# Optimization experiments

Measured on AMD Instinct MI355X. Metric: run time of the kernel, lower is better.

## Reference

```python
import jax, jax.numpy as jnp
import numpy as np

EMB, DK, DV = 768, 256, 256
B, N = 8, 2048


def setup_inputs() -> dict:
    key = jax.random.key(0)
    ks = jax.random.split(key, 9)
    s = 1.0 / np.sqrt(EMB)
    # Stack the 3 per-head Linear layers into [3, EMB, D] weights (same math).
    Wq = jax.random.uniform(ks[0], (3, EMB, DK), jnp.float32, -s, s)
    bq = jax.random.uniform(ks[1], (3, DK), jnp.float32, -s, s)
    Wk = jax.random.uniform(ks[2], (3, EMB, DK), jnp.float32, -s, s)
    bk = jax.random.uniform(ks[3], (3, DK), jnp.float32, -s, s)
    Wv = jax.random.uniform(ks[4], (3, EMB, DV), jnp.float32, -s, s)
    bv = jax.random.uniform(ks[5], (3, DV), jnp.float32, -s, s)
    s0 = 1.0 / np.sqrt(3 * DV)
    W0 = jax.random.uniform(ks[6], (3 * DV, EMB), jnp.float32, -s0, s0)
    b0 = jax.random.uniform(ks[7], (EMB,), jnp.float32, -s0, s0)
    x = jax.random.normal(ks[8], (B, N, EMB), jnp.float32)
    return {"x": x, "Wq": Wq, "bq": bq, "Wk": Wk, "bk": bk,
            "Wv": Wv, "bv": bv, "W0": W0, "b0": b0}


def reference(x, Wq, bq, Wk, bk, Wv, bv, W0, b0):
    # QKV for all 3 heads in one batched GEMM each: [B,3,N,D]
    Q = jnp.einsum('bne,hed->bhnd', x, Wq) + bq[None, :, None, :]
    K = jnp.einsum('bne,hed->bhnd', x, Wk) + bk[None, :, None, :]
    V = jnp.einsum('bne,hed->bhnd', x, Wv) + bv[None, :, None, :]
    scores = jnp.einsum('bhnd,bhmd->bhnm', Q, K) / jnp.sqrt(jnp.float32(DK))
    attn = jax.nn.softmax(scores, axis=-1)
    res = jnp.einsum('bhnm,bhmd->bhnd', attn, V)  # [B,3,N,DV]
    # concat heads along feature dim (head order matches torch concat order)
    res = jnp.transpose(res, (0, 2, 1, 3)).reshape(B, N, 3 * DV)
    return res @ W0 + b0
```

## Files before the change

### kernel.cpp

```cpp
#include <hip/hip_runtime.h>
#include <stdint.h>

typedef __attribute__((ext_vector_type(8))) short short8;
typedef __attribute__((ext_vector_type(4))) float floatx4;

#define EMB 768
#define DKV 256
#define NB  8
#define NS  2048

__device__ __forceinline__ float b2f(unsigned short u) {
  union { unsigned int i; float f; } v; v.i = ((unsigned int)u) << 16; return v.f;
}
__device__ __forceinline__ unsigned short f2b(float f) {
  union { float f; unsigned int i; } v; v.f = f;
  return (unsigned short)((v.i + 0x7FFFu + ((v.i >> 16) & 1u)) >> 16);
}

__device__ __forceinline__ short8 load8x(const void* p, size_t e, int f32) {
  short8 r;
  if (f32) {
    const float* f = (const float*)p + e;
    float4 a = *(const float4*)f;
    float4 b = *(const float4*)(f + 4);
    r[0] = (short)f2b(a.x); r[1] = (short)f2b(a.y);
    r[2] = (short)f2b(a.z); r[3] = (short)f2b(a.w);
    r[4] = (short)f2b(b.x); r[5] = (short)f2b(b.y);
    r[6] = (short)f2b(b.z); r[7] = (short)f2b(b.w);
  } else {
    r = *(const short8*)((const unsigned short*)p + e);
  }
  return r;
}
__device__ __forceinline__ float loadf(const void* p, size_t e, int f32) {
  return f32 ? ((const float*)p)[e] : b2f(((const unsigned short*)p)[e]);
}

__global__ __launch_bounds__(256) void detect_kernel(
    const unsigned short* __restrict__ x, int* __restrict__ flag) {
  __shared__ int cnt;
  if (threadIdx.x == 0) cnt = 0;
  __syncthreads();
  int bad = 0;
  for (int i = threadIdx.x; i < 1024; i += 256) {
    float v = b2f(x[i]);
    if (!(fabsf(v) <= 1e4f)) bad++;
  }
  atomicAdd(&cnt, bad);
  __syncthreads();
  if (threadIdx.x == 0) flag[0] = (cnt > 16) ? 1 : 0;
}

__global__ __launch_bounds__(256) void repack_wt(
    const void* __restrict__ Wq, const void* __restrict__ Wk,
    const void* __restrict__ Wv, unsigned short* __restrict__ WT,
    const int* __restrict__ flag) {
  __shared__ unsigned short tile[32][33];
  const int f32 = *flag;
  const int tid = threadIdx.x;
  const int slab = blockIdx.z;
  const int t = slab / 3, h = slab - t * 3;
  const int k0 = blockIdx.x * 32, d0 = blockIdx.y * 32;
  const void* Wsrc = (t == 0) ? Wq : ((t == 1) ? Wk : Wv);
#pragma unroll
  for (int rr = 0; rr < 4; ++rr) {
    int ki = rr * 8 + (tid >> 5), di = tid & 31;
    tile[ki][di] = f2b(loadf(Wsrc, (size_t)(h * EMB + k0 + ki) * DKV + d0 + di, f32));
  }
  __syncthreads();
#pragma unroll
  for (int rr = 0; rr < 4; ++rr) {
    int di = rr * 8 + (tid >> 5), ki = tid & 31;
    WT[(size_t)(slab * 256 + d0 + di) * EMB + k0 + ki] = tile[ki][di];
  }
}

__global__ __launch_bounds__(256) void repack_w0t(
    const void* __restrict__ W0, unsigned short* __restrict__ W0T,
    const int* __restrict__ flag) {
  __shared__ unsigned short tile[32][33];
  const int f32 = *flag;
  const int tid = threadIdx.x;
  const int k0 = blockIdx.x * 32, o0 = blockIdx.y * 32;
#pragma unroll
  for (int rr = 0; rr < 4; ++rr) {
    int ki = rr * 8 + (tid >> 5), oi = tid & 31;
    tile[ki][oi] = f2b(loadf(W0, (size_t)(k0 + ki) * EMB + o0 + oi, f32));
  }
  __syncthreads();
#pragma unroll
  for (int rr = 0; rr < 4; ++rr) {
    int oi = rr * 8 + (tid >> 5), ki = tid & 31;
    W0T[(size_t)(o0 + oi) * EMB + k0 + ki] = tile[ki][oi];
  }
}

__global__ __launch_bounds__(256, 2) void kv_gemm(
    const void* __restrict__ X, const unsigned short* __restrict__ WT,
    const void* __restrict__ bk, const void* __restrict__ bv,
    unsigned short* __restrict__ Kb, unsigned short* __restrict__ Vtb,
    const int* __restrict__ flag) {
  __shared__ __align__(16) unsigned short As[128 * 40];
  __shared__ __align__(16) unsigned short BsK[128 * 40];
  __shared__ __align__(16) unsigned short BsV[128 * 40];
  const int f32 = *flag;
  const int tid = threadIdx.x;
  const int wave = tid >> 6, lane = tid & 63, quad = lane >> 4, l15 = lane & 15;
  const int wm = wave >> 1, wn = wave & 1;
  const int row0 = blockIdx.y * 128;
  const int cb = blockIdx.x * 128;

  floatx4 accK[4][4], accV[4][4];
  for (int m = 0; m < 4; ++m)
    for (int n = 0; n < 4; ++n) { accK[m][n] = (floatx4)0.0f; accV[m][n] = (floatx4)0.0f; }

  const size_t arow0 = (size_t)row0 * EMB;
  const unsigned short* BbK = WT + (size_t)(768 + cb) * EMB;
  const unsigned short* BbV = WT + (size_t)(1536 + cb) * EMB;

  for (int k0 = 0; k0 < EMB; k0 += 32) {
    short8 va[2], vk[2], vv[2];
#pragma unroll
    for (int i = 0; i < 2; ++i) {
      int idx = i * 256 + tid;
      int r = idx >> 2, kp = (idx & 3) << 3;
      va[i] = load8x(X, arow0 + (size_t)r * EMB + k0 + kp, f32);
      vk[i] = *(const short8*)(BbK + (size_t)r * EMB + k0 + kp);
      vv[i] = *(const short8*)(BbV + (size_t)r * EMB + k0 + kp);
    }
    __syncthreads();
#pragma unroll
    for (int i = 0; i < 2; ++i) {
      int idx = i * 256 + tid;
      int off = (idx >> 2) * 40 + (idx & 3) * 8;
      *(short8*)&As[off] = va[i];
      *(short8*)&BsK[off] = vk[i];
      *(short8*)&BsV[off] = vv[i];
    }
    __syncthreads();
    short8 af[4], bk4[4], bv4[4];
#pragma unroll
    for (int m = 0; m < 4; ++m)
      af[m] = *(const short8*)&As[(wm * 64 + m * 16 + l15) * 40 + quad * 8];
#pragma unroll
    for (int n = 0; n < 4; ++n) {
      bk4[n] = *(const short8*)&BsK[(wn * 64 + n * 16 + l15) * 40 + quad * 8];
      bv4[n] = *(const short8*)&BsV[(wn * 64 + n * 16 + l15) * 40 + quad * 8];
    }
#pragma unroll
    for (int n = 0; n < 4; ++n)
#pragma unroll
      for (int m = 0; m < 4; ++m) {
        accK[m][n] = __builtin_amdgcn_mfma_f32_16x16x32_bf16(af[m], bk4[n], accK[m][n], 0, 0, 0);
        accV[m][n] = __builtin_amdgcn_mfma_f32_16x16x32_bf16(af[m], bv4[n], accV[m][n], 0, 0, 0);
      }
  }

  const int h = cb >> 8;
  const int dbase = cb & 255;

#pragma unroll
  for (int n = 0; n < 4; ++n) {
    const int cc = wn * 64 + n * 16 + l15;
    const float bvv = loadf(bk, h * 256 + dbase + cc, f32);
    const int d = dbase + cc;
#pragma unroll
    for (int m = 0; m < 4; ++m) {
      const int rbase = row0 + wm * 64 + m * 16 + quad * 4;
#pragma unroll
      for (int r = 0; r < 4; ++r) {
        const int row = rbase + r;
        const int bb = row >> 11, nn = row & 2047;
        Kb[((size_t)(bb * 3 + h) * 2048 + nn) * 256 + d] = f2b(accK[m][n][r] + bvv);
      }
    }
  }
#pragma unroll
  for (int n = 0; n < 4; ++n) {
    const int cc = wn * 64 + n * 16 + l15;
    const float bvv = loadf(bv, h * 256 + dbase + cc, f32);
    const int d = dbase + cc;
#pragma unroll
    for (int m = 0; m < 4; ++m) {
      const int rbase = row0 + wm * 64 + m * 16 + quad * 4;
      const int bb = rbase >> 11, nn = rbase & 2047;
      const size_t base = ((size_t)(bb * 3 + h) * 256 + d) * 2048 + nn;
      uint2 val;
      val.x = (uint32_t)f2b(accV[m][n][0] + bvv) | ((uint32_t)f2b(accV[m][n][1] + bvv) << 16);
      val.y = (uint32_t)f2b(accV[m][n][2] + bvv) | ((uint32_t)f2b(accV[m][n][3] + bvv) << 16);
      *(uint2*)(Vtb + base) = val;
    }
  }
}

__global__ __launch_bounds__(256, 3) void flash_fused(
    const void* __restrict__ X, const unsigned short* __restrict__ WT,
    const void* __restrict__ bq,
    const unsigned short* __restrict__ Kb, const unsigned short* __restrict__ Vtb,
    unsigned short* __restrict__ Ob, const int* __restrict__ flag) {
  __shared__ __align__(16) unsigned short smem[21248];
  unsigned short* AsQ = smem;
  unsigned short* BsQ = smem + 2560;
  unsigned short* Qs  = smem;
  unsigned short* Ks  = smem;
  unsigned short* Vts = smem + 8448;
  unsigned short* Ps  = smem + 18688;

  const int f32 = *flag;
  const int tid = threadIdx.x;
  const int wave = tid >> 6, lane = tid & 63, quad = lane >> 4, l15 = lane & 15;
  const int bh = blockIdx.x;
  const int bb = bh / 3, hh = bh - bb * 3;
  const int q0 = blockIdx.y * 64;

  short8 qf[8];

  {
    const size_t xrow0 = (size_t)bb * NS + q0;
    floatx4 qacc[4][4];
    for (int m = 0; m < 4; ++m)
      for (int n = 0; n < 4; ++n) qacc[m][n] = (floatx4)0.0f;

    for (int k0 = 0; k0 < EMB; k0 += 32) {
      short8 va, vb[4];
      {
        int r = tid >> 2, kp = (tid & 3) << 3;
        va = load8x(X, (xrow0 + r) * EMB + k0 + kp, f32);
      }
#pragma unroll
      for (int i = 0; i < 4; ++i) {
        int c = i * 256 + tid;
        int n = c >> 2, kp = (c & 3) << 3;
        vb[i] = *(const short8*)(WT + (size_t)(hh * 256 + n) * EMB + k0 + kp);
      }
      __syncthreads();
      *(short8*)&AsQ[(tid >> 2) * 40 + (tid & 3) * 8] = va;
#pragma unroll
      for (int i = 0; i < 4; ++i) {
        int c = i * 256 + tid;
        *(short8*)&BsQ[(c >> 2) * 40 + (c & 3) * 8] = vb[i];
      }
      __syncthreads();
      short8 af[4], bf[4];
#pragma unroll
      for (int m = 0; m < 4; ++m)
        af[m] = *(const short8*)&AsQ[(m * 16 + l15) * 40 + quad * 8];
#pragma unroll
      for (int n = 0; n < 4; ++n)
        bf[n] = *(const short8*)&BsQ[(wave * 64 + n * 16 + l15) * 40 + quad * 8];
#pragma unroll
      for (int n = 0; n < 4; ++n)
#pragma unroll
        for (int m = 0; m < 4; ++m)
          qacc[m][n] = __builtin_amdgcn_mfma_f32_16x16x32_bf16(af[m], bf[n], qacc[m][n], 0, 0, 0);
    }
    __syncthreads();

#pragma unroll
    for (int n = 0; n < 4; ++n) {
      const int col = wave * 64 + n * 16 + l15;
      const float bqv = loadf(bq, hh * 256 + col, f32);
#pragma unroll
      for (int m = 0; m < 4; ++m)
#pragma unroll
        for (int r = 0; r < 4; ++r)
          Qs[(m * 16 + quad * 4 + r) * 264 + col] = f2b((qacc[m][n][r] + bqv) * 0.0625f);
    }
    __syncthreads();
#pragma unroll
    for (int ks = 0; ks < 8; ++ks)
      qf[ks] = *(const short8*)&Qs[(wave * 16 + l15) * 264 + ks * 32 + quad * 8];
    __syncthreads();
  }

  const unsigned short* Kp = Kb + (size_t)bh * NS * DKV;
  const unsigned short* Vp = Vtb + (size_t)bh * DKV * NS;

  floatx4 oacc[4][4];
  for (int m = 0; m < 4; ++m)
    for (int ct = 0; ct < 4; ++ct) oacc[m][ct] = (floatx4)0.0f;
  float l_part[4] = {0.f, 0.f, 0.f, 0.f};

  for (int j0 = 0; j0 < NS; j0 += 32) {
    short8 kv[4], vv[4];
#pragma unroll
    for (int i = 0; i < 4; ++i) {
      int c = i * 256 + tid;
      kv[i] = *(const short8*)(Kp + (size_t)(j0 + (c >> 5)) * DKV + ((c & 31) << 3));
      vv[i] = *(const short8*)(Vp + (size_t)(c >> 2) * NS + j0 + ((c & 3) << 3));
    }
    __syncthreads();
#pragma unroll
    for (int i = 0; i < 4; ++i) {
      int c = i * 256 + tid;
      *(short8*)&Ks[(c >> 5) * 264 + (c & 31) * 8] = kv[i];
      *(short8*)&Vts[(c >> 2) * 40 + (c & 3) * 8] = vv[i];
    }
    __syncthreads();

    floatx4 sacc[2];
    sacc[0] = (floatx4)0.0f; sacc[1] = (floatx4)0.0f;
    __builtin_amdgcn_s_setprio(1);
#pragma unroll
    for (int ks = 0; ks < 8; ++ks)
#pragma unroll
      for (int ct = 0; ct < 2; ++ct) {
        short8 bfr = *(const short8*)&Ks[(ct * 16 + l15) * 264 + ks * 32 + quad * 8];
        sacc[ct] = __builtin_amdgcn_mfma_f32_16x16x32_bf16(qf[ks], bfr, sacc[ct], 0, 0, 0);
      }
    __builtin_amdgcn_s_setprio(0);

#pragma unroll
    for (int ct = 0; ct < 2; ++ct)
#pragma unroll
      for (int r = 0; r < 4; ++r) {
        float p = __expf(sacc[ct][r]);
        l_part[r] += p;
        Ps[(wave * 16 + quad * 4 + r) * 40 + ct * 16 + l15] = f2b(p);
      }
    __syncthreads();

    short8 pa[4];
#pragma unroll
    for (int m = 0; m < 4; ++m)
      pa[m] = *(const short8*)&Ps[(m * 16 + l15) * 40 + quad * 8];
    __builtin_amdgcn_s_setprio(1);
#pragma unroll
    for (int ct = 0; ct < 4; ++ct) {
      short8 vb = *(const short8*)&Vts[(wave * 64 + ct * 16 + l15) * 40 + quad * 8];
#pragma unroll
      for (int m = 0; m < 4; ++m)
        oacc[m][ct] = __builtin_amdgcn_mfma_f32_16x16x32_bf16(pa[m], vb, oacc[m][ct], 0, 0, 0);
    }
    __builtin_amdgcn_s_setprio(0);
  }

  float l_r[4];
#pragma unroll
  for (int r = 0; r < 4; ++r) l_r[r] = l_part[r];
#pragma unroll
  for (int mask = 1; mask < 16; mask <<= 1)
#pragma unroll
    for (int r = 0; r < 4; ++r) l_r[r] += __shfl_xor(l_r[r], mask);

  __syncthreads();
  float* Lsf = (float*)smem;
  if (l15 == 0) {
#pragma unroll
    for (int r = 0; r < 4; ++r) Lsf[wave * 16 + quad * 4 + r] = l_r[r];
  }
  __syncthreads();

#pragma unroll
  for (int m = 0; m < 4; ++m) {
    float linv[4];
#pragma unroll
    for (int r = 0; r < 4; ++r) linv[r] = 1.0f / Lsf[m * 16 + quad * 4 + r];
#pragma unroll
    for (int ct = 0; ct < 4; ++ct) {
      const int col = hh * DKV + wave * 64 + ct * 16 + l15;
#pragma unroll
      for (int r = 0; r < 4; ++r) {
        const int n = q0 + m * 16 + quad * 4 + r;
        Ob[((size_t)(bb * NS + n)) * EMB + col] = f2b(oacc[m][ct][r] * linv[r]);
      }
    }
  }
}

__global__ __launch_bounds__(256) void out_gemm(
    const unsigned short* __restrict__ A, const unsigned short* __restrict__ W0T,
    const void* __restrict__ b0, void* __restrict__ out,
    const int* __restrict__ flag) {
  __shared__ __align__(16) unsigned short As[128 * 40];
  __shared__ __align__(16) unsigned short Bs[128 * 40];
  const int f32 = *flag;
  const int tid = threadIdx.x;
  const int wave = tid >> 6, lane = tid & 63, quad = lane >> 4, l15 = lane & 15;
  const int wm = wave >> 1, wn = wave & 1;
  const int row0 = blockIdx.y * 128;
  const int c0 = blockIdx.x * 128;

  floatx4 acc[4][4];
  for (int m = 0; m < 4; ++m)
    for (int n = 0; n < 4; ++n) acc[m][n] = (floatx4)0.0f;

  const unsigned short* Ab = A + (size_t)row0 * EMB;
  const unsigned short* Bb = W0T + (size_t)c0 * EMB;

  for (int k0 = 0; k0 < EMB; k0 += 32) {
    short8 va[2], vb[2];
#pragma unroll
    for (int i = 0; i < 2; ++i) {
      int idx = i * 256 + tid;
      int r = idx >> 2, kp = (idx & 3) << 3;
      va[i] = *(const short8*)(Ab + (size_t)r * EMB + k0 + kp);
      vb[i] = *(const short8*)(Bb + (size_t)r * EMB + k0 + kp);
    }
    __syncthreads();
#pragma unroll
    for (int i = 0; i < 2; ++i) {
      int idx = i * 256 + tid;
      *(short8*)&As[(idx >> 2) * 40 + (idx & 3) * 8] = va[i];
      *(short8*)&Bs[(idx >> 2) * 40 + (idx & 3) * 8] = vb[i];
    }
    __syncthreads();
    short8 af[4], bf[4];
#pragma unroll
    for (int m = 0; m < 4; ++m)
      af[m] = *(const short8*)&As[(wm * 64 + m * 16 + l15) * 40 + quad * 8];
#pragma unroll
    for (int n = 0; n < 4; ++n)
      bf[n] = *(const short8*)&Bs[(wn * 64 + n * 16 + l15) * 40 + quad * 8];
#pragma unroll
    for (int n = 0; n < 4; ++n)
#pragma unroll
      for (int m = 0; m < 4; ++m)
        acc[m][n] = __builtin_amdgcn_mfma_f32_16x16x32_bf16(af[m], bf[n], acc[m][n], 0, 0, 0);
  }

#pragma unroll
  for (int n = 0; n < 4; ++n) {
    const int col = c0 + wn * 64 + n * 16 + l15;
    const float bvv = loadf(b0, col, f32);
#pragma unroll
    for (int m = 0; m < 4; ++m) {
      const int rbase = row0 + wm * 64 + m * 16 + quad * 4;
#pragma unroll
      for (int r = 0; r < 4; ++r) {
        const float v = acc[m][n][r] + bvv;
        const size_t idx = (size_t)(rbase + r) * EMB + col;
        if (f32) ((float*)out)[idx] = v;
        else     ((unsigned short*)out)[idx] = f2b(v);
      }
    }
  }
}

extern "C" void kernel_launch(void* const* d_in, const int* in_sizes, int n_in,
                              void* d_out, int out_size, void* d_ws, size_t ws_size,
                              hipStream_t stream) {
  const void* x  = d_in[0];
  const void* Wq = d_in[1];
  const void* bq = d_in[2];
  const void* Wk = d_in[3];
  const void* bk = d_in[4];
  const void* Wv = d_in[5];
  const void* bv = d_in[6];
  const void* W0 = d_in[7];
  const void* b0 = d_in[8];

  unsigned short* ws = (unsigned short*)d_ws;
  const size_t SZ = (size_t)NB * 3 * NS * DKV;
  unsigned short* Kb  = (unsigned short*)d_out;
  unsigned short* Vtb = ws;
  unsigned short* Ob  = ws + SZ;
  unsigned short* WT  = ws + 2 * SZ;
  unsigned short* W0T = WT + (size_t)2304 * EMB;
  int* flag = (int*)(W0T + (size_t)EMB * EMB);

  detect_kernel<<<dim3(1), dim3(256), 0, stream>>>((const unsigned short*)x, flag);
  repack_wt<<<dim3(24, 8, 9), dim3(256), 0, stream>>>(Wq, Wk, Wv, WT, flag);
  repack_w0t<<<dim3(24, 24), dim3(256), 0, stream>>>(W0, W0T, flag);
  kv_gemm<<<dim3(6, 128), dim3(256), 0, stream>>>(x, WT, bk, bv, Kb, Vtb, flag);
  flash_fused<<<dim3(24, 32), dim3(256), 0, stream>>>(x, WT, bq, Kb, Vtb, Ob, flag);
  out_gemm<<<dim3(6, 128), dim3(256), 0, stream>>>(Ob, W0T, b0, d_out, flag);
}
```

Before: 449.1 us.

## Prefetch next K-tile into registers across all GEMM and attention loops

Applies register double-buffering to the KV projection GEMM, the Q projection, the attention K/V streaming loop and the output projection. Each loop now issues global loads for the next tile right after storing the current tile to LDS, so memory latency overlaps with the MFMA work. The attention loop moves its barrier to the end of each iteration so LDS is not overwritten early. It also raises wave priority around MFMA blocks. This costs extra live registers, which may lower occupancy.

```diff
diff --git a/kernel.cpp b/kernel.cpp
--- a/kernel.cpp
+++ b/kernel.cpp
@@ -118,16 +118,17 @@
   const unsigned short* BbK = WT + (size_t)(768 + cb) * EMB;
   const unsigned short* BbV = WT + (size_t)(1536 + cb) * EMB;
 
+  short8 va[2], vk[2], vv[2];
+#pragma unroll
+  for (int i = 0; i < 2; ++i) {
+    int idx = i * 256 + tid;
+    int r = idx >> 2, kp = (idx & 3) << 3;
+    va[i] = load8x(X, arow0 + (size_t)r * EMB + kp, f32);
+    vk[i] = *(const short8*)(BbK + (size_t)r * EMB + kp);
+    vv[i] = *(const short8*)(BbV + (size_t)r * EMB + kp);
+  }
+
   for (int k0 = 0; k0 < EMB; k0 += 32) {
-    short8 va[2], vk[2], vv[2];
-#pragma unroll
-    for (int i = 0; i < 2; ++i) {
-      int idx = i * 256 + tid;
-      int r = idx >> 2, kp = (idx & 3) << 3;
-      va[i] = load8x(X, arow0 + (size_t)r * EMB + k0 + kp, f32);
-      vk[i] = *(const short8*)(BbK + (size_t)r * EMB + k0 + kp);
-      vv[i] = *(const short8*)(BbV + (size_t)r * EMB + k0 + kp);
-    }
     __syncthreads();
 #pragma unroll
     for (int i = 0; i < 2; ++i) {
@@ -137,6 +138,17 @@
       *(short8*)&BsK[off] = vk[i];
       *(short8*)&BsV[off] = vv[i];
     }
+    if (k0 + 32 < EMB) {
+      const int kn = k0 + 32;
+#pragma unroll
+      for (int i = 0; i < 2; ++i) {
+        int idx = i * 256 + tid;
+        int r = idx >> 2, kp = (idx & 3) << 3;
+        va[i] = load8x(X, arow0 + (size_t)r * EMB + kn + kp, f32);
+        vk[i] = *(const short8*)(BbK + (size_t)r * EMB + kn + kp);
+        vv[i] = *(const short8*)(BbV + (size_t)r * EMB + kn + kp);
+      }
+    }
     __syncthreads();
     short8 af[4], bk4[4], bv4[4];
 #pragma unroll
@@ -147,6 +159,7 @@
       bk4[n] = *(const short8*)&BsK[(wn * 64 + n * 16 + l15) * 40 + quad * 8];
       bv4[n] = *(const short8*)&BsV[(wn * 64 + n * 16 + l15) * 40 + quad * 8];
     }
+    __builtin_amdgcn_s_setprio(1);
 #pragma unroll
     for (int n = 0; n < 4; ++n)
 #pragma unroll
@@ -154,6 +167,7 @@
         accK[m][n] = __builtin_amdgcn_mfma_f32_16x16x32_bf16(af[m], bk4[n], accK[m][n], 0, 0, 0);
         accV[m][n] = __builtin_amdgcn_mfma_f32_16x16x32_bf16(af[m], bv4[n], accV[m][n], 0, 0, 0);
       }
+    __builtin_amdgcn_s_setprio(0);
   }
 
   const int h = cb >> 8;
@@ -213,7 +227,11 @@
   const int bb = bh / 3, hh = bh - bb * 3;
   const int q0 = blockIdx.y * 64;
 
+  const unsigned short* Kp = Kb + (size_t)bh * NS * DKV;
+  const unsigned short* Vp = Vtb + (size_t)bh * DKV * NS;
+
   short8 qf[8];
+  short8 kv[4], vv[4];
 
   {
     const size_t xrow0 = (size_t)bb * NS + q0;
@@ -221,18 +239,18 @@
     for (int m = 0; m < 4; ++m)
       for (int n = 0; n < 4; ++n) qacc[m][n] = (floatx4)0.0f;
 
+    short8 va, vb[4];
+    {
+      int r = tid >> 2, kp = (tid & 3) << 3;
+      va = load8x(X, (xrow0 + r) * EMB + kp, f32);
+    }
+#pragma unroll
+    for (int i = 0; i < 4; ++i) {
+      int c = i * 256 + tid;
+      vb[i] = *(const short8*)(WT + (size_t)(hh * 256 + (c >> 2)) * EMB + ((c & 3) << 3));
+    }
+
     for (int k0 = 0; k0 < EMB; k0 += 32) {
-      short8 va, vb[4];
-      {
-        int r = tid >> 2, kp = (tid & 3) << 3;
-        va = load8x(X, (xrow0 + r) * EMB + k0 + kp, f32);
-      }
-#pragma unroll
-      for (int i = 0; i < 4; ++i) {
-        int c = i * 256 + tid;
-        int n = c >> 2, kp = (c & 3) << 3;
-        vb[i] = *(const short8*)(WT + (size_t)(hh * 256 + n) * EMB + k0 + kp);
-      }
       __syncthreads();
       *(short8*)&AsQ[(tid >> 2) * 40 + (tid & 3) * 8] = va;
 #pragma unroll
@@ -240,6 +258,18 @@
         int c = i * 256 + tid;
         *(short8*)&BsQ[(c >> 2) * 40 + (c & 3) * 8] = vb[i];
       }
+      if (k0 + 32 < EMB) {
+        const int kn = k0 + 32;
+        {
+          int r = tid >> 2, kp = (tid & 3) << 3;
+          va = load8x(X, (xrow0 + r) * EMB + kn + kp, f32);
+        }
+#pragma unroll
+        for (int i = 0; i < 4; ++i) {
+          int c = i * 256 + tid;
+          vb[i] = *(const short8*)(WT + (size_t)(hh * 256 + (c >> 2)) * EMB + kn + ((c & 3) << 3));
+        }
+      }
       __syncthreads();
       short8 af[4], bf[4];
 #pragma unroll
@@ -248,13 +278,22 @@
 #pragma unroll
       for (int n = 0; n < 4; ++n)
         bf[n] = *(const short8*)&BsQ[(wave * 64 + n * 16 + l15) * 40 + quad * 8];
+      __builtin_amdgcn_s_setprio(1);
 #pragma unroll
       for (int n = 0; n < 4; ++n)
 #pragma unroll
         for (int m = 0; m < 4; ++m)
           qacc[m][n] = __builtin_amdgcn_mfma_f32_16x16x32_bf16(af[m], bf[n], qacc[m][n], 0, 0, 0);
-    }
-    __syncthreads();
+      __builtin_amdgcn_s_setprio(0);
+    }
+    __syncthreads();
+
+#pragma unroll
+    for (int i = 0; i < 4; ++i) {
+      int c = i * 256 + tid;
+      kv[i] = *(const short8*)(Kp + (size_t)(c >> 5) * DKV + ((c & 31) << 3));
+      vv[i] = *(const short8*)(Vp + (size_t)(c >> 2) * NS + ((c & 3) << 3));
+    }
 
 #pragma unroll
     for (int n = 0; n < 4; ++n) {
@@ -272,9 +311,6 @@
       qf[ks] = *(const short8*)&Qs[(wave * 16 + l15) * 264 + ks * 32 + quad * 8];
     __syncthreads();
   }
-
-  const unsigned short* Kp = Kb + (size_t)bh * NS * DKV;
-  const unsigned short* Vp = Vtb + (size_t)bh * DKV * NS;
 
   floatx4 oacc[4][4];
   for (int m = 0; m < 4; ++m)
@@ -282,20 +318,21 @@
   float l_part[4] = {0.f, 0.f, 0.f, 0.f};
 
   for (int j0 = 0; j0 < NS; j0 += 32) {
-    short8 kv[4], vv[4];
-#pragma unroll
-    for (int i = 0; i < 4; ++i) {
-      int c = i * 256 + tid;
-      kv[i] = *(const short8*)(Kp + (size_t)(j0 + (c >> 5)) * DKV + ((c & 31) << 3));
-      vv[i] = *(const short8*)(Vp + (size_t)(c >> 2) * NS + j0 + ((c & 3) << 3));
-    }
-    __syncthreads();
 #pragma unroll
     for (int i = 0; i < 4; ++i) {
       int c = i * 256 + tid;
       *(short8*)&Ks[(c >> 5) * 264 + (c & 31) * 8] = kv[i];
       *(short8*)&Vts[(c >> 2) * 40 + (c & 3) * 8] = vv[i];
     }
+    if (j0 + 32 < NS) {
+      const int jn = j0 + 32;
+#pragma unroll
+      for (int i = 0; i < 4; ++i) {
+        int c = i * 256 + tid;
+        kv[i] = *(const short8*)(Kp + (size_t)(jn + (c >> 5)) * DKV + ((c & 31) << 3));
+        vv[i] = *(const short8*)(Vp + (size_t)(c >> 2) * NS + jn + ((c & 3) << 3));
+      }
+    }
     __syncthreads();
 
     floatx4 sacc[2];
@@ -333,6 +370,7 @@
         oacc[m][ct] = __builtin_amdgcn_mfma_f32_16x16x32_bf16(pa[m], vb, oacc[m][ct], 0, 0, 0);
     }
     __builtin_amdgcn_s_setprio(0);
+    __syncthreads();
   }
 
   float l_r[4];
@@ -343,7 +381,6 @@
 #pragma unroll
     for (int r = 0; r < 4; ++r) l_r[r] += __shfl_xor(l_r[r], mask);
 
-  __syncthreads();
   float* Lsf = (float*)smem;
   if (l15 == 0) {
 #pragma unroll
@@ -388,15 +425,16 @@
   const unsigned short* Ab = A + (size_t)row0 * EMB;
   const unsigned short* Bb = W0T + (size_t)c0 * EMB;
 
+  short8 va[2], vb[2];
+#pragma unroll
+  for (int i = 0; i < 2; ++i) {
+    int idx = i * 256 + tid;
+    int r = idx >> 2, kp = (idx & 3) << 3;
+    va[i] = *(const short8*)(Ab + (size_t)r * EMB + kp);
+    vb[i] = *(const short8*)(Bb + (size_t)r * EMB + kp);
+  }
+
   for (int k0 = 0; k0 < EMB; k0 += 32) {
-    short8 va[2], vb[2];
-#pragma unroll
-    for (int i = 0; i < 2; ++i) {
-      int idx = i * 256 + tid;
-      int r = idx >> 2, kp = (idx & 3) << 3;
-      va[i] = *(const short8*)(Ab + (size_t)r * EMB + k0 + kp);
-      vb[i] = *(const short8*)(Bb + (size_t)r * EMB + k0 + kp);
-    }
     __syncthreads();
 #pragma unroll
     for (int i = 0; i < 2; ++i) {
@@ -404,6 +442,16 @@
       *(short8*)&As[(idx >> 2) * 40 + (idx & 3) * 8] = va[i];
       *(short8*)&Bs[(idx >> 2) * 40 + (idx & 3) * 8] = vb[i];
     }
+    if (k0 + 32 < EMB) {
+      const int kn = k0 + 32;
+#pragma unroll
+      for (int i = 0; i < 2; ++i) {
+        int idx = i * 256 + tid;
+        int r = idx >> 2, kp = (idx & 3) << 3;
+        va[i] = *(const short8*)(Ab + (size_t)r * EMB + kn + kp);
+        vb[i] = *(const short8*)(Bb + (size_t)r * EMB + kn + kp);
+      }
+    }
     __syncthreads();
     short8 af[4], bf[4];
 #pragma unroll
@@ -412,11 +460,13 @@
 #pragma unroll
     for (int n = 0; n < 4; ++n)
       bf[n] = *(const short8*)&Bs[(wn * 64 + n * 16 + l15) * 40 + quad * 8];
+    __builtin_amdgcn_s_setprio(1);
 #pragma unroll
     for (int n = 0; n < 4; ++n)
 #pragma unroll
       for (int m = 0; m < 4; ++m)
         acc[m][n] = __builtin_amdgcn_mfma_f32_16x16x32_bf16(af[m], bf[n], acc[m][n], 0, 0, 0);
+    __builtin_amdgcn_s_setprio(0);
   }
 
 #pragma unroll
```

Result: slower. 537.0 us (+19.6%).
